# Optimization experiments

Hardware: AMD Instinct MI355X
Metric: run time of the kernel (lower is better)

## Reference

```python
import jax, jax.numpy as jnp
import numpy as np

VOCAB = 32000
D = 512
H = 8
B = 1
SEQ = 4096
CHUNK = 1024  # max_len == chunk size


def _pe(seq, d):
    pos = np.arange(seq, dtype=np.float32)[:, None]
    div = np.exp(np.arange(0, d, 2, dtype=np.float32) * (-np.log(10000.0) / d))
    pe = np.zeros((seq, d), dtype=np.float32)
    pe[:, 0::2] = np.sin(pos * div)
    pe[:, 1::2] = np.cos(pos * div)
    return jnp.asarray(pe)


def _mha(x, w_in, b_in, w_out, b_out, h):
    # x: (..., L, d); attention along L, batched over leading dims.
    lead = x.shape[:-2]
    L, d = x.shape[-2], x.shape[-1]
    hd = d // h
    qkv = x @ w_in.T + b_in                      # (..., L, 3d)
    q, k, v = jnp.split(qkv, 3, axis=-1)
    q = q.reshape(lead + (L, h, hd))
    k = k.reshape(lead + (L, h, hd))
    v = v.reshape(lead + (L, h, hd))
    scores = jnp.einsum('...qhd,...khd->...hqk', q, k) * (1.0 / np.sqrt(hd))
    attn = jax.nn.softmax(scores, axis=-1)
    o = jnp.einsum('...hqk,...khd->...qhd', attn, v).reshape(lead + (L, d))
    return o @ w_out.T + b_out


def _ln(x, g, b, eps=1e-5):
    m = x.mean(-1, keepdims=True)
    v = x.var(-1, keepdims=True)
    return (x - m) / jnp.sqrt(v + eps) * g + b


def setup_inputs() -> dict:
    key = jax.random.key(0)
    ks = jax.random.split(key, 10)
    n = lambda k, s: jax.random.normal(k, s, jnp.float32) * 0.02
    return {
        'tokens': jax.random.randint(ks[0], (B, SEQ), 0, VOCAB),
        'emb': n(ks[1], (VOCAB, D)),
        'chunk_w_in': n(ks[2], (3 * D, D)), 'chunk_b_in': jnp.zeros((3 * D,), jnp.float32),
        'chunk_w_out': n(ks[3], (D, D)), 'chunk_b_out': jnp.zeros((D,), jnp.float32),
        'glob_w_in': n(ks[4], (3 * D, D)), 'glob_b_in': jnp.zeros((3 * D,), jnp.float32),
        'glob_w_out': n(ks[5], (D, D)), 'glob_b_out': jnp.zeros((D,), jnp.float32),
        'ln1_g': jnp.ones((D,), jnp.float32), 'ln1_b': jnp.zeros((D,), jnp.float32),
        'ffn_w1': n(ks[6], (4 * D, D)), 'ffn_b1': jnp.zeros((4 * D,), jnp.float32),
        'ffn_w2': n(ks[7], (D, 4 * D)), 'ffn_b2': jnp.zeros((D,), jnp.float32),
        'ln2_g': jnp.ones((D,), jnp.float32), 'ln2_b': jnp.zeros((D,), jnp.float32),
        'fc_w': n(ks[8], (VOCAB, D)), 'fc_b': jnp.zeros((VOCAB,), jnp.float32),
    }


def reference(tokens, emb, chunk_w_in, chunk_b_in, chunk_w_out, chunk_b_out,
              glob_w_in, glob_b_in, glob_w_out, glob_b_out,
              ln1_g, ln1_b, ffn_w1, ffn_b1, ffn_w2, ffn_b2,
              ln2_g, ln2_b, fc_w, fc_b):
    # embedding * sqrt(d) + sinusoidal positional encoding (dropout in eval = identity)
    x = emb[tokens] * np.sqrt(D).astype(np.float32) + _pe(SEQ, D)[None]  # (B, S, d)
    b, s, d = x.shape
    nc = s // CHUNK
    # BeamSplitter chunk stage: attend across the nc chunks at each intra-chunk position
    xc = x.reshape(b, nc, CHUNK, d).transpose(0, 2, 1, 3)   # (B, CHUNK, nc, d)
    ca = _mha(xc, chunk_w_in, chunk_b_in, chunk_w_out, chunk_b_out, H)
    ca = ca.transpose(0, 2, 1, 3).reshape(b, s, d)          # (B, S, d)
    # global stage: full attention over the sequence
    ga = _mha(ca, glob_w_in, glob_b_in, glob_w_out, glob_b_out, H)
    # post-norm transformer encoder layer
    x = _ln(x + ga, ln1_g, ln1_b)
    f = jax.nn.relu(x @ ffn_w1.T + ffn_b1) @ ffn_w2.T + ffn_b2
    x = _ln(x + f, ln2_g, ln2_b)
    return x @ fc_w.T + fc_b                                 # (B, S, VOCAB)
```

## Files before the change

kernel.cpp:

```cpp
#include <hip/hip_runtime.h>

typedef __attribute__((ext_vector_type(8))) short bf16x8;
typedef __attribute__((ext_vector_type(4))) float f32x4;
typedef unsigned short u16;

__device__ __forceinline__ u16 f2b(float f) {
  union { float f; unsigned u; } v; v.f = f;
  return (u16)((v.u + 0x7FFFu + ((v.u >> 16) & 1u)) >> 16);
}
__device__ __forceinline__ float b2f(u16 x) {
  union { unsigned u; float f; } v; v.u = (unsigned)x << 16; return v.f;
}

__device__ __forceinline__ void gload16(const void* g, void* l) {
  __builtin_amdgcn_global_load_lds((__attribute__((address_space(1))) void*)(g),
                                   (__attribute__((address_space(3))) void*)(l),
                                   16, 0, 0);
}

__device__ __forceinline__ void mbar() {
  asm volatile("" ::: "memory");
  __builtin_amdgcn_s_barrier();
  asm volatile("" ::: "memory");
}

__device__ __forceinline__ void cv1(const float4* __restrict__ s, u16* __restrict__ d, int i) {
  float4 v = s[i];
  unsigned long long pk = (unsigned long long)f2b(v.x) |
                          ((unsigned long long)f2b(v.y) << 16) |
                          ((unsigned long long)f2b(v.z) << 32) |
                          ((unsigned long long)f2b(v.w) << 48);
  *(unsigned long long*)(d + (size_t)i * 4) = pk;
}

__global__ __launch_bounds__(256)
void f2b_multi(const float4* s0, u16* d0, const float4* s1, u16* d1,
               const float4* s2, u16* d2, const float4* s3, u16* d3,
               const float4* s4, u16* d4, const float4* s5, u16* d5,
               const float4* s6, u16* d6) {
  int i = blockIdx.x * 256 + threadIdx.x;
  const int stride = gridDim.x * 256;
  for (; i < 5144576; i += stride) {
    int j = i;
    if (j < 196608) { cv1(s0, d0, j); continue; }
    j -= 196608;
    if (j < 65536) { cv1(s1, d1, j); continue; }
    j -= 65536;
    if (j < 196608) { cv1(s2, d2, j); continue; }
    j -= 196608;
    if (j < 65536) { cv1(s3, d3, j); continue; }
    j -= 65536;
    if (j < 262144) { cv1(s4, d4, j); continue; }
    j -= 262144;
    if (j < 262144) { cv1(s5, d5, j); continue; }
    j -= 262144;
    cv1(s6, d6, j);
  }
}

__global__ __launch_bounds__(256) void embed_pe(const int* __restrict__ tok,
    const float* __restrict__ emb, float* __restrict__ xf, u16* __restrict__ xb) {
  const int s = blockIdx.x;
  const int i = threadIdx.x;
  const int t = tok[s];
  const float div = __expf((float)(2 * i) * -0.017988946039015984f);
  const float ang = (float)s * div;
  const float sv = __sinf(ang), cv = __cosf(ang);
  const float* e = emb + (size_t)t * 512 + 2 * i;
  const float x0 = e[0] * 22.627416997969522f + sv;
  const float x1 = e[1] * 22.627416997969522f + cv;
  const size_t o = (size_t)s * 512 + 2 * i;
  xf[o] = x0; xf[o + 1] = x1;
  xb[o] = f2b(x0); xb[o + 1] = f2b(x1);
}

template<int BM, int RELU, int WF32, int WB16>
__global__ __launch_bounds__(256)
void gemm_bt(const u16* __restrict__ A, const u16* __restrict__ B,
             const float* __restrict__ bias, float* __restrict__ Cf,
             u16* __restrict__ Cb, int M, int N, int K)
{
  constexpr int MFR = BM / 32;
  __shared__ __align__(16) u16 As[BM * 64];
  __shared__ __align__(16) u16 Bs[128 * 64];
  const int tid = threadIdx.x;
  const int wid = tid >> 6, lane = tid & 63;
  const int lo = lane & 15, hi = lane >> 4;
  const int nbn = N >> 7;
  const int cpx = (int)gridDim.x >> 3;
  const int bid = blockIdx.x;
  const int swz = (bid & 7) * cpx + (bid >> 3);
  const int bi = swz / nbn, bj = swz - bi * nbn;
  const size_t row0 = (size_t)bi * BM, col0 = (size_t)bj << 7;
  const int wr = (wid >> 1) * (BM / 2), wc = (wid & 1) << 6;
  const int srow = (wid << 3) + (lane >> 3);
  const int scol = ((lane & 7) ^ (lane >> 3)) << 3;

  f32x4 acc[MFR][4] = {};

  auto rdA = [&](int row, int ks) -> bf16x8 {
    return *(const bf16x8*)((const char*)As + row * 128 + ((((ks << 2) | hi) ^ (row & 7)) << 4));
  };
  auto rdB = [&](int row, int ks) -> bf16x8 {
    return *(const bf16x8*)((const char*)Bs + row * 128 + ((((ks << 2) | hi) ^ (row & 7)) << 4));
  };

  for (int k0 = 0; k0 < K; k0 += 64) {
    __syncthreads();
#pragma unroll
    for (int p = 0; p < BM / 32; ++p)
      gload16(A + (row0 + srow + 32 * p) * (size_t)K + k0 + scol, &As[(wid * 8 + 32 * p) * 64]);
#pragma unroll
    for (int p = 0; p < 4; ++p)
      gload16(B + (col0 + srow + 32 * p) * (size_t)K + k0 + scol, &Bs[(wid * 8 + 32 * p) * 64]);
    __syncthreads();
#pragma unroll
    for (int ks = 0; ks < 2; ++ks) {
      bf16x8 af[MFR], bfr[4];
#pragma unroll
      for (int m = 0; m < MFR; ++m) af[m] = rdA(wr + m * 16 + lo, ks);
#pragma unroll
      for (int n = 0; n < 4; ++n) bfr[n] = rdB(wc + n * 16 + lo, ks);
#pragma unroll
      for (int m = 0; m < MFR; ++m)
#pragma unroll
        for (int n = 0; n < 4; ++n)
          acc[m][n] = __builtin_amdgcn_mfma_f32_16x16x32_bf16(af[m], bfr[n], acc[m][n], 0, 0, 0);
    }
  }

#pragma unroll
  for (int m = 0; m < MFR; ++m)
#pragma unroll
    for (int n = 0; n < 4; ++n) {
      const size_t c = col0 + wc + n * 16 + lo;
      const float bv = bias[c];
#pragma unroll
      for (int i = 0; i < 4; ++i) {
        const size_t r = row0 + wr + m * 16 + hi * 4 + i;
        float v = acc[m][n][i] + bv;
        if (RELU) v = fmaxf(v, 0.0f);
        if (WF32) Cf[r * (size_t)N + c] = v;
        if (WB16) Cb[r * (size_t)N + c] = f2b(v);
      }
    }
}

template<int KC>
__global__ __launch_bounds__(512, 2)
void gemm256p(const u16* __restrict__ A, const u16* __restrict__ B,
              const float* __restrict__ bias, float* __restrict__ C, int N)
{
  __shared__ __align__(16) u16 LA[2][256 * 64];
  __shared__ __align__(16) u16 LB[2][256 * 64];
  const int tid = threadIdx.x;
  const int wid = tid >> 6, lane = tid & 63;
  const int lo = lane & 15, hi = lane >> 4;
  const int b = blockIdx.x;
  const int bj = b % 125, bi0 = b / 125;
  const size_t col0 = (size_t)bj << 8;
  const int wrow = (wid >> 2) << 7;
  const int wcol = (wid & 3) << 6;

  const int srow = (wid << 3) + (lane >> 3);
  const int scol = ((lane & 7) ^ (lane >> 3)) << 3;
  const u16* srcB = B + (col0 + srow) * (size_t)KC + scol;
  const int ldst = wid << 9;

  float bv[4];
#pragma unroll
  for (int n = 0; n < 4; ++n) bv[n] = bias[col0 + wcol + n * 16 + lo];
  asm volatile("" : "+v"(bv[0]), "+v"(bv[1]), "+v"(bv[2]), "+v"(bv[3]));

  f32x4 acc[8][4] = {};

  auto stageAB = [&](int s) {
    const int jj = s >> 3, tt = s & 7, buf = s & 1;
    const u16* sA = A + ((size_t)((bi0 + 2 * jj) << 8) + srow) * KC + tt * 64 + scol;
#pragma unroll
    for (int i = 0; i < 4; ++i)
      gload16(sA + (size_t)(i * 64) * KC, &LA[buf][ldst + i * 4096]);
    const u16* sB = srcB + tt * 64;
#pragma unroll
    for (int i = 0; i < 4; ++i)
      gload16(sB + (size_t)(i * 64) * KC, &LB[buf][ldst + i * 4096]);
  };

  auto rd = [&](const u16* base, int row, int ks) -> bf16x8 {
    const int byte = row * 128 + ((((ks << 2) | hi) ^ (row & 7)) << 4);
    return *(const bf16x8*)((const char*)base + byte);
  };

  stageAB(0);
  stageAB(1);

  for (int j = 0; j < 8; ++j) {
#pragma unroll
    for (int t = 0; t < 8; ++t) {
      const int s = j * 8 + t;
      const u16* Ab = LA[s & 1];
      const u16* Bb = LB[s & 1];
      if (j > 0 && t <= 1)  { asm volatile("s_waitcnt vmcnt(40)" ::: "memory"); }
      else if (s == 63)     { asm volatile("s_waitcnt vmcnt(0)" ::: "memory"); }
      else                  { asm volatile("s_waitcnt vmcnt(8)" ::: "memory"); }
      __builtin_amdgcn_sched_barrier(0);
      mbar();

      bf16x8 afr[4], bfr[4];
#pragma unroll
      for (int ks = 0; ks < 2; ++ks) {
#pragma unroll
        for (int m = 0; m < 4; ++m) afr[m] = rd(Ab, wrow + m * 16 + lo, ks);
#pragma unroll
        for (int n = 0; n < 4; ++n) bfr[n] = rd(Bb, wcol + n * 16 + lo, ks);
        mbar();
        asm volatile("s_waitcnt lgkmcnt(0)" ::: "memory");
        __builtin_amdgcn_sched_barrier(0);
        __builtin_amdgcn_s_setprio(1);
#pragma unroll
        for (int m = 0; m < 4; ++m)
#pragma unroll
          for (int n = 0; n < 4; ++n)
            acc[m][n] = __builtin_amdgcn_mfma_f32_16x16x32_bf16(afr[m], bfr[n], acc[m][n], 0, 0, 0);
        __builtin_amdgcn_s_setprio(0);
        mbar();
#pragma unroll
        for (int m = 0; m < 4; ++m) afr[m] = rd(Ab, wrow + (4 + m) * 16 + lo, ks);
        mbar();
        asm volatile("s_waitcnt lgkmcnt(0)" ::: "memory");
        __builtin_amdgcn_sched_barrier(0);
        __builtin_amdgcn_s_setprio(1);
#pragma unroll
        for (int m = 0; m < 4; ++m)
#pragma unroll
          for (int n = 0; n < 4; ++n)
            acc[4 + m][n] = __builtin_amdgcn_mfma_f32_16x16x32_bf16(afr[m], bfr[n], acc[4 + m][n], 0, 0, 0);
        __builtin_amdgcn_s_setprio(0);
        mbar();
      }
      if (s + 2 < 64) stageAB(s + 2);
    }
    const size_t row0 = (size_t)((bi0 + 2 * j) << 8);
#pragma unroll
    for (int m = 0; m < 8; ++m)
#pragma unroll
      for (int n = 0; n < 4; ++n) {
        const size_t c = col0 + wcol + n * 16 + lo;
#pragma unroll
        for (int i = 0; i < 4; ++i) {
          const size_t r = row0 + wrow + m * 16 + hi * 4 + i;
          C[r * (size_t)N + c] = acc[m][n][i] + bv[n];
        }
      }
#pragma unroll
    for (int m = 0; m < 8; ++m)
#pragma unroll
      for (int n = 0; n < 4; ++n)
        acc[m][n] = f32x4{0.f, 0.f, 0.f, 0.f};
  }
}

__global__ __launch_bounds__(64)
void chunk_attn(const u16* __restrict__ qkv, u16* __restrict__ out) {
  const int p = blockIdx.x, h = blockIdx.y, d = threadIdx.x;
  float q[4], k[4], v[4];
#pragma unroll
  for (int c = 0; c < 4; ++c) {
    const u16* b = qkv + (size_t)((c << 10) + p) * 1536 + (h << 6) + d;
    q[c] = b2f(b[0]); k[c] = b2f(b[512]); v[c] = b2f(b[1024]);
  }
  float sc[4][4];
#pragma unroll
  for (int i = 0; i < 4; ++i)
#pragma unroll
    for (int j = 0; j < 4; ++j) sc[i][j] = q[i] * k[j];
#pragma unroll
  for (int mask = 1; mask < 64; mask <<= 1)
#pragma unroll
    for (int i = 0; i < 4; ++i)
#pragma unroll
      for (int j = 0; j < 4; ++j) sc[i][j] += __shfl_xor(sc[i][j], mask);
#pragma unroll
  for (int i = 0; i < 4; ++i) {
    float s0 = sc[i][0] * 0.125f, s1 = sc[i][1] * 0.125f,
          s2 = sc[i][2] * 0.125f, s3 = sc[i][3] * 0.125f;
    const float mx = fmaxf(fmaxf(s0, s1), fmaxf(s2, s3));
    const float e0 = __expf(s0 - mx), e1 = __expf(s1 - mx),
                e2 = __expf(s2 - mx), e3 = __expf(s3 - mx);
    const float inv = 1.0f / (e0 + e1 + e2 + e3);
    const float o = (e0 * v[0] + e1 * v[1] + e2 * v[2] + e3 * v[3]) * inv;
    out[(size_t)((i << 10) + p) * 512 + (h << 6) + d] = f2b(o);
  }
}

__global__ __launch_bounds__(512, 4)
void flash_attn(const u16* __restrict__ qkv, float* __restrict__ pO,
                float* __restrict__ pm, float* __restrict__ pl) {
  __shared__ __align__(16) u16 Ks[64 * 64];
  __shared__ __align__(16) u16 Vt[64 * 64];
  __shared__ __align__(16) u16 Pp[8][16 * 64];
  const int tid = threadIdx.x, wid = tid >> 6, lane = tid & 63;
  const int lo = lane & 15, hi = lane >> 4;
  const int q0 = blockIdx.x << 7, h = blockIdx.y, z = blockIdx.z;
  const int kvb = z << 11;
  const int hoff = h << 6;
  char* KsB = (char*)Ks; char* VtB = (char*)Vt;
  char* Pw = (char*)&Pp[wid][0];
  const int xsw = (lo & 7) << 4;
  constexpr float C1 = 0.18033688011112042f;

  bf16x8 qf[2];
#pragma unroll
  for (int kh = 0; kh < 2; ++kh)
    qf[kh] = *(const bf16x8*)(qkv + (size_t)(q0 + wid * 16 + lo) * 1536 + hoff + kh * 32 + hi * 8);

  f32x4 o[4] = {};
  float mr = -3e38f, lr = 0.f;

  const int krow = tid >> 3, kq = tid & 7;

  bf16x8 kpre = *(const bf16x8*)(qkv + (size_t)(kvb + krow) * 1536 + 512 + hoff + kq * 8);
  bf16x8 vpre = *(const bf16x8*)(qkv + (size_t)(kvb + krow) * 1536 + 1024 + hoff + kq * 8);

  for (int kv0 = kvb; kv0 < kvb + 2048; kv0 += 64) {
    __syncthreads();
    *(bf16x8*)(KsB + ((krow * 128 + kq * 16) ^ ((krow & 7) << 4))) = kpre;
    {
      const unsigned* vp = (const unsigned*)&vpre;
      const int oddr = krow & 1;
      const unsigned t0 = oddr ? vp[0] : vp[2];
      const unsigned t1 = oddr ? vp[1] : vp[3];
      const unsigned r0 = (unsigned)__shfl_xor((int)t0, 8);
      const unsigned r1 = (unsigned)__shfl_xor((int)t1, 8);
      const unsigned E0 = oddr ? r0 : vp[0];
      const unsigned E1 = oddr ? r1 : vp[1];
      const unsigned O0 = oddr ? vp[2] : r0;
      const unsigned O1 = oddr ? vp[3] : r1;
      const int jp = krow & ~1;
      const int db = kq * 8 + oddr * 4;
      unsigned w0 = (E0 & 0xffffu) | (O0 << 16);
      unsigned w1 = (E0 >> 16) | (O0 & 0xffff0000u);
      unsigned w2 = (E1 & 0xffffu) | (O1 << 16);
      unsigned w3 = (E1 >> 16) | (O1 & 0xffff0000u);
      *(unsigned*)(VtB + (((db + 0) * 128 + 2 * jp) ^ (((db + 0) & 7) << 4))) = w0;
      *(unsigned*)(VtB + (((db + 1) * 128 + 2 * jp) ^ (((db + 1) & 7) << 4))) = w1;
      *(unsigned*)(VtB + (((db + 2) * 128 + 2 * jp) ^ (((db + 2) & 7) << 4))) = w2;
      *(unsigned*)(VtB + (((db + 3) * 128 + 2 * jp) ^ (((db + 3) & 7) << 4))) = w3;
    }
    __syncthreads();
    if (kv0 + 64 < kvb + 2048) {
      kpre = *(const bf16x8*)(qkv + (size_t)(kv0 + 64 + krow) * 1536 + 512 + hoff + kq * 8);
      vpre = *(const bf16x8*)(qkv + (size_t)(kv0 + 64 + krow) * 1536 + 1024 + hoff + kq * 8);
    }

    f32x4 s[4] = {};
#pragma unroll
    for (int n = 0; n < 4; ++n) {
      const int key = n * 16 + lo;
#pragma unroll
      for (int kh = 0; kh < 2; ++kh) {
        bf16x8 kf = *(const bf16x8*)(KsB + ((key * 128 + kh * 64 + hi * 16) ^ ((key & 7) << 4)));
        s[n] = __builtin_amdgcn_mfma_f32_16x16x32_bf16(kf, qf[kh], s[n], 0, 0, 0);
      }
    }

    float pmx = s[0][0];
#pragma unroll
    for (int n = 0; n < 4; ++n)
#pragma unroll
      for (int i = 0; i < 4; ++i) pmx = fmaxf(pmx, s[n][i]);
    pmx = fmaxf(pmx, __shfl_xor(pmx, 16));
    pmx = fmaxf(pmx, __shfl_xor(pmx, 32));

    if (__any(pmx > mr + 64.f)) {
      const float mn = fmaxf(mr, pmx);
      const float sc = exp2f((mr - mn) * C1);
      mr = mn;
      lr *= sc;
#pragma unroll
      for (int i = 0; i < 4; ++i) {
        const float sq = __shfl(sc, hi * 4 + i);
#pragma unroll
        for (int n = 0; n < 4; ++n) o[n][i] *= sq;
      }
    }

    const float mc = mr * C1;
    float rs = 0.f;
    unsigned U[8];
#pragma unroll
    for (int n = 0; n < 4; ++n) {
      const float p0 = exp2f(fmaf(s[n][0], C1, -mc));
      const float p1 = exp2f(fmaf(s[n][1], C1, -mc));
      const float p2 = exp2f(fmaf(s[n][2], C1, -mc));
      const float p3 = exp2f(fmaf(s[n][3], C1, -mc));
      rs += (p0 + p1) + (p2 + p3);
      asm("v_cvt_pk_bf16_f32 %0, %1, %2" : "=v"(U[2 * n])     : "v"(p0), "v"(p1));
      asm("v_cvt_pk_bf16_f32 %0, %1, %2" : "=v"(U[2 * n + 1]) : "v"(p2), "v"(p3));
    }
    rs += __shfl_xor(rs, 16);
    rs += __shfl_xor(rs, 32);
    lr += rs;
#pragma unroll
    for (int n = 0; n < 4; ++n) {
      const int off = lo * 128 + ((n * 32 + hi * 8) ^ xsw);
      const unsigned long long dw = (unsigned long long)U[2 * n] |
                                    ((unsigned long long)U[2 * n + 1] << 32);
      *(unsigned long long*)(Pw + off) = dw;
    }

#pragma unroll
    for (int kh = 0; kh < 2; ++kh) {
      bf16x8 pa = *(const bf16x8*)(Pw + lo * 128 + ((kh * 64 + hi * 16) ^ xsw));
#pragma unroll
      for (int n = 0; n < 4; ++n) {
        const int vd = n * 16 + lo;
        bf16x8 vf = *(const bf16x8*)(VtB + ((vd * 128 + kh * 64 + hi * 16) ^ ((vd & 7) << 4)));
        o[n] = __builtin_amdgcn_mfma_f32_16x16x32_bf16(pa, vf, o[n], 0, 0, 0);
      }
    }
  }

#pragma unroll
  for (int i = 0; i < 4; ++i) {
    const int r = q0 + wid * 16 + hi * 4 + i;
#pragma unroll
    for (int n = 0; n < 4; ++n)
      pO[((size_t)z * 4096 + r) * 512 + hoff + n * 16 + lo] = o[n][i];
  }
  if (hi == 0) {
    const int r = q0 + wid * 16 + lo;
    pm[(z * 8 + h) * 4096 + r] = mr;
    pl[(z * 8 + h) * 4096 + r] = lr;
  }
}

__global__ __launch_bounds__(256)
void attn_merge(const float* __restrict__ pO, const float* __restrict__ pm,
                const float* __restrict__ pl, u16* __restrict__ out) {
  constexpr float C1 = 0.18033688011112042f;
  const int tid = threadIdx.x, lane = tid & 63, w = tid >> 6;
  const int row = blockIdx.x * 4 + w;
  const int d = lane * 8, h = lane >> 3;
  const float m0 = pm[h * 4096 + row], m1 = pm[(8 + h) * 4096 + row];
  const float l0 = pl[h * 4096 + row], l1 = pl[(8 + h) * 4096 + row];
  const float M = fmaxf(m0, m1);
  const float w0 = exp2f((m0 - M) * C1), w1 = exp2f((m1 - M) * C1);
  const float inv = 1.0f / (l0 * w0 + l1 * w1);
  const float* a = pO + (size_t)row * 512 + d;
  const float* b = pO + ((size_t)4096 + row) * 512 + d;
  float4 a0 = *(const float4*)a, a1 = *(const float4*)(a + 4);
  float4 b0 = *(const float4*)b, b1 = *(const float4*)(b + 4);
  const float A[8] = {a0.x, a0.y, a0.z, a0.w, a1.x, a1.y, a1.z, a1.w};
  const float Bv[8] = {b0.x, b0.y, b0.z, b0.w, b1.x, b1.y, b1.z, b1.w};
#pragma unroll
  for (int j = 0; j < 8; ++j)
    out[(size_t)row * 512 + d + j] = f2b((A[j] * w0 + Bv[j] * w1) * inv);
}

__global__ __launch_bounds__(256)
void add_ln(const float* __restrict__ a, const float* __restrict__ b,
            const float* __restrict__ g, const float* __restrict__ be,
            float* __restrict__ of, u16* __restrict__ ob) {
  const int wid = threadIdx.x >> 6, lane = threadIdx.x & 63;
  const int row = blockIdx.x * 4 + wid;
  const size_t base = (size_t)row * 512 + lane * 8;
  float4 a0 = *(const float4*)(a + base), a1 = *(const float4*)(a + base + 4);
  float4 b0 = *(const float4*)(b + base), b1 = *(const float4*)(b + base + 4);
  float x[8] = {a0.x + b0.x, a0.y + b0.y, a0.z + b0.z, a0.w + b0.w,
                a1.x + b1.x, a1.y + b1.y, a1.z + b1.z, a1.w + b1.w};
  float s = 0.f, sq = 0.f;
#pragma unroll
  for (int j = 0; j < 8; ++j) { s += x[j]; sq += x[j] * x[j]; }
#pragma unroll
  for (int mask = 1; mask < 64; mask <<= 1) {
    s += __shfl_xor(s, mask);
    sq += __shfl_xor(sq, mask);
  }
  const float mean = s * (1.0f / 512.0f);
  const float var = sq * (1.0f / 512.0f) - mean * mean;
  const float rstd = rsqrtf(var + 1e-5f);
  float4 g0 = *(const float4*)(g + lane * 8), g1 = *(const float4*)(g + lane * 8 + 4);
  float4 e0 = *(const float4*)(be + lane * 8), e1 = *(const float4*)(be + lane * 8 + 4);
  const float gg[8] = {g0.x, g0.y, g0.z, g0.w, g1.x, g1.y, g1.z, g1.w};
  const float bb[8] = {e0.x, e0.y, e0.z, e0.w, e1.x, e1.y, e1.z, e1.w};
#pragma unroll
  for (int j = 0; j < 8; ++j) {
    const float y = (x[j] - mean) * rstd * gg[j] + bb[j];
    of[base + j] = y;
    ob[base + j] = f2b(y);
  }
}

extern "C" void kernel_launch(void* const* d_in, const int* in_sizes, int n_in,
                              void* d_out, int out_size, void* d_ws, size_t ws_size,
                              hipStream_t stream) {
  (void)in_sizes; (void)n_in; (void)out_size; (void)ws_size;
  const int*   tokens = (const int*)d_in[0];
  const float* emb    = (const float*)d_in[1];
  const float* cwin   = (const float*)d_in[2];
  const float* cbin   = (const float*)d_in[3];
  const float* cwout  = (const float*)d_in[4];
  const float* cbout  = (const float*)d_in[5];
  const float* gwin   = (const float*)d_in[6];
  const float* gbin   = (const float*)d_in[7];
  const float* gwout  = (const float*)d_in[8];
  const float* gbout  = (const float*)d_in[9];
  const float* ln1g   = (const float*)d_in[10];
  const float* ln1b   = (const float*)d_in[11];
  const float* fw1    = (const float*)d_in[12];
  const float* fb1    = (const float*)d_in[13];
  const float* fw2    = (const float*)d_in[14];
  const float* fb2    = (const float*)d_in[15];
  const float* ln2g   = (const float*)d_in[16];
  const float* ln2b   = (const float*)d_in[17];
  const float* fcw    = (const float*)d_in[18];
  const float* fcb    = (const float*)d_in[19];
  float* out = (float*)d_out;

  char* ws = (char*)d_ws;
  size_t off = 0;
  auto alloc = [&](size_t bytes) -> void* {
    void* p = ws + off;
    off += (bytes + 255) & ~(size_t)255;
    return p;
  };
  u16*   xb    = (u16*)alloc((size_t)4096 * 512 * 2);
  float* xf    = (float*)alloc((size_t)4096 * 512 * 4);
  u16*   qkv1b = (u16*)alloc((size_t)4096 * 1536 * 2);
  u16*   at1   = (u16*)alloc((size_t)4096 * 512 * 2);
  u16*   cab   = (u16*)alloc((size_t)4096 * 512 * 2);
  u16*   qkv2  = (u16*)alloc((size_t)4096 * 1536 * 2);
  u16*   at2   = (u16*)alloc((size_t)4096 * 512 * 2);
  float* gaf   = (float*)alloc((size_t)4096 * 512 * 4);
  float* x1f   = (float*)alloc((size_t)4096 * 512 * 4);
  u16*   x1b   = (u16*)alloc((size_t)4096 * 512 * 2);
  u16*   f1b   = (u16*)alloc((size_t)4096 * 2048 * 2);
  float* ff    = (float*)alloc((size_t)4096 * 512 * 4);
  float* x2f   = (float*)alloc((size_t)4096 * 512 * 4);
  u16*   x2b   = (u16*)alloc((size_t)4096 * 512 * 2);
  u16*   wcinb  = (u16*)alloc((size_t)1536 * 512 * 2);
  u16*   wcoutb = (u16*)alloc((size_t)512 * 512 * 2);
  u16*   wginb  = (u16*)alloc((size_t)1536 * 512 * 2);
  u16*   wgoutb = (u16*)alloc((size_t)512 * 512 * 2);
  u16*   wf1b   = (u16*)alloc((size_t)2048 * 512 * 2);
  u16*   wf2b   = (u16*)alloc((size_t)512 * 2048 * 2);
  u16*   wfcb   = (u16*)alloc((size_t)32000 * 512 * 2);

  float* pO = (float*)qkv1b;
  float* pm = (float*)xb;
  float* pl = pm + 2 * 8 * 4096;

  f2b_multi<<<2048, 256, 0, stream>>>(
      (const float4*)cwin, wcinb, (const float4*)cwout, wcoutb,
      (const float4*)gwin, wginb, (const float4*)gwout, wgoutb,
      (const float4*)fw1, wf1b, (const float4*)fw2, wf2b,
      (const float4*)fcw, wfcb);

  embed_pe<<<4096, 256, 0, stream>>>(tokens, emb, xf, xb);

  gemm_bt<128, 0, 0, 1><<<384, 256, 0, stream>>>(xb, wcinb, cbin, (float*)nullptr, qkv1b, 4096, 1536, 512);
  chunk_attn<<<dim3(1024, 8), 64, 0, stream>>>(qkv1b, at1);
  gemm_bt<64, 0, 0, 1><<<256, 256, 0, stream>>>(at1, wcoutb, cbout, (float*)nullptr, cab, 4096, 512, 512);

  gemm_bt<128, 0, 0, 1><<<384, 256, 0, stream>>>(cab, wginb, gbin, (float*)nullptr, qkv2, 4096, 1536, 512);
  flash_attn<<<dim3(32, 8, 2), 512, 0, stream>>>(qkv2, pO, pm, pl);
  attn_merge<<<1024, 256, 0, stream>>>(pO, pm, pl, at2);
  gemm_bt<64, 0, 1, 0><<<256, 256, 0, stream>>>(at2, wgoutb, gbout, gaf, (u16*)nullptr, 4096, 512, 512);

  add_ln<<<1024, 256, 0, stream>>>(xf, gaf, ln1g, ln1b, x1f, x1b);
  gemm_bt<128, 1, 0, 1><<<512, 256, 0, stream>>>(x1b, wf1b, fb1, (float*)nullptr, f1b, 4096, 2048, 512);
  gemm_bt<64, 0, 1, 0><<<256, 256, 0, stream>>>(f1b, wf2b, fb2, ff, (u16*)nullptr, 4096, 512, 2048);
  add_ln<<<1024, 256, 0, stream>>>(x1f, ff, ln2g, ln2b, x2f, x2b);

  gemm256p<512><<<250, 512, 0, stream>>>(x2b, wfcb, fcb, out, 32000);
}
```

Measured before the change: 494.2 us.

## Drop split-KV in global flash attention and remove merge kernel

The global flash attention kernel no longer splits the 4096 keys into two halves across blockIdx.z. Each block now walks the full key range and normalizes its output directly to bf16, so the fp32 partial buffers and the separate attn_merge kernel are gone. This removes a launch and the fp32 partial write/read traffic. The cost is half as many blocks (256 instead of 512 on a 256-CU part), a serial loop twice as long, and a dropped occupancy hint in launch_bounds.

```diff
diff --git a/kernel.cpp b/kernel.cpp
--- a/kernel.cpp
+++ b/kernel.cpp
@@ -293,16 +293,14 @@
   }
 }
 
-__global__ __launch_bounds__(512, 4)
-void flash_attn(const u16* __restrict__ qkv, float* __restrict__ pO,
-                float* __restrict__ pm, float* __restrict__ pl) {
+__global__ __launch_bounds__(512)
+void flash_attn(const u16* __restrict__ qkv, u16* __restrict__ out) {
   __shared__ __align__(16) u16 Ks[64 * 64];
   __shared__ __align__(16) u16 Vt[64 * 64];
   __shared__ __align__(16) u16 Pp[8][16 * 64];
   const int tid = threadIdx.x, wid = tid >> 6, lane = tid & 63;
   const int lo = lane & 15, hi = lane >> 4;
-  const int q0 = blockIdx.x << 7, h = blockIdx.y, z = blockIdx.z;
-  const int kvb = z << 11;
+  const int q0 = blockIdx.x << 7, h = blockIdx.y;
   const int hoff = h << 6;
   char* KsB = (char*)Ks; char* VtB = (char*)Vt;
   char* Pw = (char*)&Pp[wid][0];
@@ -319,10 +317,10 @@
 
   const int krow = tid >> 3, kq = tid & 7;
 
-  bf16x8 kpre = *(const bf16x8*)(qkv + (size_t)(kvb + krow) * 1536 + 512 + hoff + kq * 8);
-  bf16x8 vpre = *(const bf16x8*)(qkv + (size_t)(kvb + krow) * 1536 + 1024 + hoff + kq * 8);
-
-  for (int kv0 = kvb; kv0 < kvb + 2048; kv0 += 64) {
+  bf16x8 kpre = *(const bf16x8*)(qkv + (size_t)krow * 1536 + 512 + hoff + kq * 8);
+  bf16x8 vpre = *(const bf16x8*)(qkv + (size_t)krow * 1536 + 1024 + hoff + kq * 8);
+
+  for (int kv0 = 0; kv0 < 4096; kv0 += 64) {
     __syncthreads();
     *(bf16x8*)(KsB + ((krow * 128 + kq * 16) ^ ((krow & 7) << 4))) = kpre;
     {
@@ -348,7 +346,7 @@
       *(unsigned*)(VtB + (((db + 3) * 128 + 2 * jp) ^ (((db + 3) & 7) << 4))) = w3;
     }
     __syncthreads();
-    if (kv0 + 64 < kvb + 2048) {
+    if (kv0 + 64 < 4096) {
       kpre = *(const bf16x8*)(qkv + (size_t)(kv0 + 64 + krow) * 1536 + 512 + hoff + kq * 8);
       vpre = *(const bf16x8*)(qkv + (size_t)(kv0 + 64 + krow) * 1536 + 1024 + hoff + kq * 8);
     }
@@ -423,39 +421,13 @@
 
 #pragma unroll
   for (int i = 0; i < 4; ++i) {
+    const float lq = __shfl(lr, hi * 4 + i);
+    const float inv = 1.0f / lq;
     const int r = q0 + wid * 16 + hi * 4 + i;
 #pragma unroll
     for (int n = 0; n < 4; ++n)
-      pO[((size_t)z * 4096 + r) * 512 + hoff + n * 16 + lo] = o[n][i];
-  }
-  if (hi == 0) {
-    const int r = q0 + wid * 16 + lo;
-    pm[(z * 8 + h) * 4096 + r] = mr;
-    pl[(z * 8 + h) * 4096 + r] = lr;
-  }
-}
-
-__global__ __launch_bounds__(256)
-void attn_merge(const float* __restrict__ pO, const float* __restrict__ pm,
-                const float* __restrict__ pl, u16* __restrict__ out) {
-  constexpr float C1 = 0.18033688011112042f;
-  const int tid = threadIdx.x, lane = tid & 63, w = tid >> 6;
-  const int row = blockIdx.x * 4 + w;
-  const int d = lane * 8, h = lane >> 3;
-  const float m0 = pm[h * 4096 + row], m1 = pm[(8 + h) * 4096 + row];
-  const float l0 = pl[h * 4096 + row], l1 = pl[(8 + h) * 4096 + row];
-  const float M = fmaxf(m0, m1);
-  const float w0 = exp2f((m0 - M) * C1), w1 = exp2f((m1 - M) * C1);
-  const float inv = 1.0f / (l0 * w0 + l1 * w1);
-  const float* a = pO + (size_t)row * 512 + d;
-  const float* b = pO + ((size_t)4096 + row) * 512 + d;
-  float4 a0 = *(const float4*)a, a1 = *(const float4*)(a + 4);
-  float4 b0 = *(const float4*)b, b1 = *(const float4*)(b + 4);
-  const float A[8] = {a0.x, a0.y, a0.z, a0.w, a1.x, a1.y, a1.z, a1.w};
-  const float Bv[8] = {b0.x, b0.y, b0.z, b0.w, b1.x, b1.y, b1.z, b1.w};
-#pragma unroll
-  for (int j = 0; j < 8; ++j)
-    out[(size_t)row * 512 + d + j] = f2b((A[j] * w0 + Bv[j] * w1) * inv);
+      out[(size_t)r * 512 + hoff + n * 16 + lo] = f2b(o[n][i] * inv);
+  }
 }
 
 __global__ __launch_bounds__(256)
@@ -547,10 +519,6 @@
   u16*   wf2b   = (u16*)alloc((size_t)512 * 2048 * 2);
   u16*   wfcb   = (u16*)alloc((size_t)32000 * 512 * 2);
 
-  float* pO = (float*)qkv1b;
-  float* pm = (float*)xb;
-  float* pl = pm + 2 * 8 * 4096;
-
   f2b_multi<<<2048, 256, 0, stream>>>(
       (const float4*)cwin, wcinb, (const float4*)cwout, wcoutb,
       (const float4*)gwin, wginb, (const float4*)gwout, wgoutb,
@@ -564,8 +532,7 @@
   gemm_bt<64, 0, 0, 1><<<256, 256, 0, stream>>>(at1, wcoutb, cbout, (float*)nullptr, cab, 4096, 512, 512);
 
   gemm_bt<128, 0, 0, 1><<<384, 256, 0, stream>>>(cab, wginb, gbin, (float*)nullptr, qkv2, 4096, 1536, 512);
-  flash_attn<<<dim3(32, 8, 2), 512, 0, stream>>>(qkv2, pO, pm, pl);
-  attn_merge<<<1024, 256, 0, stream>>>(pO, pm, pl, at2);
+  flash_attn<<<dim3(32, 8), 512, 0, stream>>>(qkv2, at2);
   gemm_bt<64, 0, 1, 0><<<256, 256, 0, stream>>>(at2, wgoutb, gbout, gaf, (u16*)nullptr, 4096, 512, 512);
 
   add_ln<<<1024, 256, 0, stream>>>(xf, gaf, ln1g, ln1b, x1f, x1b);
```

After: 502.8 us. No clear change (+1.7%).

## Replace persistent FC GEMM with one-tile-per-block grid, XCD swizzle, nontemporal stores

Applied to the files above, without the earlier changes.

The final vocab projection previously ran 250 persistent blocks, each walking 8 row tiles of 256 while reusing one B column tile and pipelining loads across tiles. It now launches 2000 blocks, one 256x256 output tile each. The block index is remapped so consecutive blocks on the same XCD cover adjacent tiles, and the fp32 logits are written with nontemporal stores to avoid polluting cache. This trades B-tile reuse and cross-tile prefetch for better load balance, plus extra pipeline prologue and epilogue cost per block.

```diff
diff --git a/kernel.cpp b/kernel.cpp
--- a/kernel.cpp
+++ b/kernel.cpp
@@ -148,42 +148,41 @@
 
 template<int KC>
 __global__ __launch_bounds__(512, 2)
-void gemm256p(const u16* __restrict__ A, const u16* __restrict__ B,
-              const float* __restrict__ bias, float* __restrict__ C, int N)
+void gemm256(const u16* __restrict__ A, const u16* __restrict__ B,
+             const float* __restrict__ bias, float* __restrict__ C,
+             int M, int N)
 {
+  constexpr int T = KC / 64;
   __shared__ __align__(16) u16 LA[2][256 * 64];
   __shared__ __align__(16) u16 LB[2][256 * 64];
   const int tid = threadIdx.x;
   const int wid = tid >> 6, lane = tid & 63;
   const int lo = lane & 15, hi = lane >> 4;
-  const int b = blockIdx.x;
-  const int bj = b % 125, bi0 = b / 125;
-  const size_t col0 = (size_t)bj << 8;
+  const int nbn = N >> 8;
+  const int cpx = (int)gridDim.x >> 3;
+  const int bid = blockIdx.x;
+  const int swz = (bid & 7) * cpx + (bid >> 3);
+  const int bi = swz / nbn, bj = swz - bi * nbn;
+  const size_t row0 = (size_t)bi << 8, col0 = (size_t)bj << 8;
   const int wrow = (wid >> 2) << 7;
   const int wcol = (wid & 3) << 6;
 
   const int srow = (wid << 3) + (lane >> 3);
   const int scol = ((lane & 7) ^ (lane >> 3)) << 3;
+  const u16* srcA = A + (row0 + srow) * (size_t)KC + scol;
   const u16* srcB = B + (col0 + srow) * (size_t)KC + scol;
   const int ldst = wid << 9;
 
-  float bv[4];
-#pragma unroll
-  for (int n = 0; n < 4; ++n) bv[n] = bias[col0 + wcol + n * 16 + lo];
-  asm volatile("" : "+v"(bv[0]), "+v"(bv[1]), "+v"(bv[2]), "+v"(bv[3]));
-
   f32x4 acc[8][4] = {};
 
-  auto stageAB = [&](int s) {
-    const int jj = s >> 3, tt = s & 7, buf = s & 1;
-    const u16* sA = A + ((size_t)((bi0 + 2 * jj) << 8) + srow) * KC + tt * 64 + scol;
+  auto stage = [&](int t, int b) {
+    const size_t ko = (size_t)t * 64;
 #pragma unroll
     for (int i = 0; i < 4; ++i)
-      gload16(sA + (size_t)(i * 64) * KC, &LA[buf][ldst + i * 4096]);
-    const u16* sB = srcB + tt * 64;
+      gload16(srcA + ko + (size_t)(i * 64) * KC, &LA[b][ldst + i * 4096]);
 #pragma unroll
     for (int i = 0; i < 4; ++i)
-      gload16(sB + (size_t)(i * 64) * KC, &LB[buf][ldst + i * 4096]);
+      gload16(srcB + ko + (size_t)(i * 64) * KC, &LB[b][ldst + i * 4096]);
   };
 
   auto rd = [&](const u16* base, int row, int ks) -> bf16x8 {
@@ -191,73 +190,65 @@
     return *(const bf16x8*)((const char*)base + byte);
   };
 
-  stageAB(0);
-  stageAB(1);
-
-  for (int j = 0; j < 8; ++j) {
-#pragma unroll
-    for (int t = 0; t < 8; ++t) {
-      const int s = j * 8 + t;
-      const u16* Ab = LA[s & 1];
-      const u16* Bb = LB[s & 1];
-      if (j > 0 && t <= 1)  { asm volatile("s_waitcnt vmcnt(40)" ::: "memory"); }
-      else if (s == 63)     { asm volatile("s_waitcnt vmcnt(0)" ::: "memory"); }
-      else                  { asm volatile("s_waitcnt vmcnt(8)" ::: "memory"); }
+  stage(0, 0);
+  stage(1, 1);
+
+  for (int t = 0; t < T; ++t) {
+    const int b = t & 1;
+    const u16* Ab = LA[b];
+    const u16* Bb = LB[b];
+    if (t + 1 < T) { asm volatile("s_waitcnt vmcnt(8)" ::: "memory"); }
+    else           { asm volatile("s_waitcnt vmcnt(0)" ::: "memory"); }
+    __builtin_amdgcn_sched_barrier(0);
+    mbar();
+
+    bf16x8 afr[4], bfr[4];
+#pragma unroll
+    for (int ks = 0; ks < 2; ++ks) {
+#pragma unroll
+      for (int m = 0; m < 4; ++m) afr[m] = rd(Ab, wrow + m * 16 + lo, ks);
+#pragma unroll
+      for (int n = 0; n < 4; ++n) bfr[n] = rd(Bb, wcol + n * 16 + lo, ks);
+      mbar();
+      asm volatile("s_waitcnt lgkmcnt(0)" ::: "memory");
       __builtin_amdgcn_sched_barrier(0);
+      __builtin_amdgcn_s_setprio(1);
+#pragma unroll
+      for (int m = 0; m < 4; ++m)
+#pragma unroll
+        for (int n = 0; n < 4; ++n)
+          acc[m][n] = __builtin_amdgcn_mfma_f32_16x16x32_bf16(afr[m], bfr[n], acc[m][n], 0, 0, 0);
+      __builtin_amdgcn_s_setprio(0);
       mbar();
-
-      bf16x8 afr[4], bfr[4];
-#pragma unroll
-      for (int ks = 0; ks < 2; ++ks) {
-#pragma unroll
-        for (int m = 0; m < 4; ++m) afr[m] = rd(Ab, wrow + m * 16 + lo, ks);
-#pragma unroll
-        for (int n = 0; n < 4; ++n) bfr[n] = rd(Bb, wcol + n * 16 + lo, ks);
-        mbar();
-        asm volatile("s_waitcnt lgkmcnt(0)" ::: "memory");
-        __builtin_amdgcn_sched_barrier(0);
-        __builtin_amdgcn_s_setprio(1);
-#pragma unroll
-        for (int m = 0; m < 4; ++m)
-#pragma unroll
-          for (int n = 0; n < 4; ++n)
-            acc[m][n] = __builtin_amdgcn_mfma_f32_16x16x32_bf16(afr[m], bfr[n], acc[m][n], 0, 0, 0);
-        __builtin_amdgcn_s_setprio(0);
-        mbar();
-#pragma unroll
-        for (int m = 0; m < 4; ++m) afr[m] = rd(Ab, wrow + (4 + m) * 16 + lo, ks);
-        mbar();
-        asm volatile("s_waitcnt lgkmcnt(0)" ::: "memory");
-        __builtin_amdgcn_sched_barrier(0);
-        __builtin_amdgcn_s_setprio(1);
-#pragma unroll
-        for (int m = 0; m < 4; ++m)
-#pragma unroll
-          for (int n = 0; n < 4; ++n)
-            acc[4 + m][n] = __builtin_amdgcn_mfma_f32_16x16x32_bf16(afr[m], bfr[n], acc[4 + m][n], 0, 0, 0);
-        __builtin_amdgcn_s_setprio(0);
-        mbar();
+#pragma unroll
+      for (int m = 0; m < 4; ++m) afr[m] = rd(Ab, wrow + (4 + m) * 16 + lo, ks);
+      mbar();
+      asm volatile("s_waitcnt lgkmcnt(0)" ::: "memory");
+      __builtin_amdgcn_sched_barrier(0);
+      __builtin_amdgcn_s_setprio(1);
+#pragma unroll
+      for (int m = 0; m < 4; ++m)
+#pragma unroll
+        for (int n = 0; n < 4; ++n)
+          acc[4 + m][n] = __builtin_amdgcn_mfma_f32_16x16x32_bf16(afr[m], bfr[n], acc[4 + m][n], 0, 0, 0);
+      __builtin_amdgcn_s_setprio(0);
+      mbar();
+    }
+    if (t + 2 < T) stage(t + 2, b);
+  }
+
+#pragma unroll
+  for (int m = 0; m < 8; ++m)
+#pragma unroll
+    for (int n = 0; n < 4; ++n) {
+      const size_t c = col0 + wcol + n * 16 + lo;
+      const float bv = bias[c];
+#pragma unroll
+      for (int i = 0; i < 4; ++i) {
+        const size_t r = row0 + wrow + m * 16 + hi * 4 + i;
+        __builtin_nontemporal_store(acc[m][n][i] + bv, &C[r * (size_t)N + c]);
       }
-      if (s + 2 < 64) stageAB(s + 2);
-    }
-    const size_t row0 = (size_t)((bi0 + 2 * j) << 8);
-#pragma unroll
-    for (int m = 0; m < 8; ++m)
-#pragma unroll
-      for (int n = 0; n < 4; ++n) {
-        const size_t c = col0 + wcol + n * 16 + lo;
-#pragma unroll
-        for (int i = 0; i < 4; ++i) {
-          const size_t r = row0 + wrow + m * 16 + hi * 4 + i;
-          C[r * (size_t)N + c] = acc[m][n][i] + bv[n];
-        }
-      }
-#pragma unroll
-    for (int m = 0; m < 8; ++m)
-#pragma unroll
-      for (int n = 0; n < 4; ++n)
-        acc[m][n] = f32x4{0.f, 0.f, 0.f, 0.f};
-  }
+    }
 }
 
 __global__ __launch_bounds__(64)
@@ -573,5 +564,5 @@
   gemm_bt<64, 0, 1, 0><<<256, 256, 0, stream>>>(f1b, wf2b, fb2, ff, (u16*)nullptr, 4096, 512, 2048);
   add_ln<<<1024, 256, 0, stream>>>(x1f, ff, ln2g, ln2b, x2f, x2b);
 
-  gemm256p<512><<<250, 512, 0, stream>>>(x2b, wfcb, fcb, out, 32000);
-}
+  gemm256<512><<<2000, 512, 0, stream>>>(x2b, wfcb, fcb, out, 4096, 32000);
+}
```

New measurement: 453.6 us. 1.09x faster.
